# Kernel optimization log

Measured on AMD Instinct MI355X. Metric: run time of the kernel, lower is better.

The kernel has to match this reference:

```python
import jax, jax.numpy as jnp
import numpy as np

MODEL_DIM = 256
PAIR_IMPORTANCE_WEIGHT = 0.5
B, S, D = 4, 4096, MODEL_DIM


def setup_inputs() -> dict:
    key = jax.random.key(0)
    ks = jax.random.split(key, 6)
    return {
        "query": jax.random.normal(ks[0], (B, S, D), dtype=jnp.float32),
        "key": jax.random.normal(ks[1], (B, S, D), dtype=jnp.float32),
        "value": jax.random.normal(ks[2], (B, S, D), dtype=jnp.float32),
        "W_query": jax.random.normal(ks[3], (D, D), dtype=jnp.float32),
        "W_key": jax.random.normal(ks[4], (D, D), dtype=jnp.float32),
        "W_value": jax.random.normal(ks[5], (D, D), dtype=jnp.float32),
    }


def reference(query, key, value, W_query, W_key, W_value):
    # Projections: [B,S,D] @ [D,D]
    q = jnp.einsum('bsd,de->bse', query, W_query)
    k = jnp.einsum('bsd,de->bse', key, W_key)
    v = jnp.einsum('bsd,de->bse', value, W_value)
    scale = jnp.sqrt(jnp.asarray(MODEL_DIM, dtype=q.dtype))
    # Full [B,S,S] score matrix (global max forces materialization)
    scores = jnp.einsum('bqd,bkd->bqk', q, k) / scale
    s_len = scores.shape[1]
    diag_bias = jnp.eye(s_len, dtype=scores.dtype) * jnp.max(scores)
    scores = scores + PAIR_IMPORTANCE_WEIGHT * diag_bias  # broadcast over batch
    attention_weights = jax.nn.softmax(scores, axis=-1)
    output = jnp.einsum('bqk,bkd->bqd', attention_weights, v)
    return output, attention_weights
```

## Files before the change

kernel.cpp:

```cpp
#include <hip/hip_runtime.h>
#include <cstdint>
#include <cstddef>

#define BB 4
#define SS 4096
#define DD 256
#define PIW 0.5f
#define NROW (BB * SS)

typedef float          f32x4  __attribute__((ext_vector_type(4)));
typedef __bf16         bf16v8 __attribute__((ext_vector_type(8)));
typedef unsigned short u16v8  __attribute__((ext_vector_type(8)));
typedef unsigned short u16v4  __attribute__((ext_vector_type(4)));

__device__ __forceinline__ f32x4 mfma_bf16(u16v8 a, u16v8 b, f32x4 c) {
    return __builtin_amdgcn_mfma_f32_16x16x32_bf16(
        __builtin_bit_cast(bf16v8, a), __builtin_bit_cast(bf16v8, b), c, 0, 0, 0);
}

__device__ __forceinline__ unsigned short f2bf(float f) {
    unsigned u = __float_as_uint(f);
    u += 0x7FFFu + ((u >> 16) & 1u);
    return (unsigned short)(u >> 16);
}
__device__ __forceinline__ float bf2f(unsigned short h) {
    return __uint_as_float(((unsigned)h) << 16);
}
__device__ __forceinline__ unsigned fenc(float x) {
    unsigned u = __float_as_uint(x);
    return (u & 0x80000000u) ? ~u : (u | 0x80000000u);
}
__device__ __forceinline__ float fdec(unsigned e) {
    return __uint_as_float((e & 0x80000000u) ? (e ^ 0x80000000u) : ~e);
}

__device__ __forceinline__ void split8(float4 x0, float4 x1, u16v8* h, u16v8* l) {
    float xs[8] = {x0.x, x0.y, x0.z, x0.w, x1.x, x1.y, x1.z, x1.w};
    #pragma unroll
    for (int e = 0; e < 8; e++) {
        unsigned short hh = f2bf(xs[e]);
        (*h)[e] = hh;
        (*l)[e] = f2bf(xs[e] - bf2f(hh));
    }
}

#define FPAD 36

__global__ __launch_bounds__(256) void proj_mfma(
    const float* __restrict__ query, const float* __restrict__ key_, const float* __restrict__ value,
    const float* __restrict__ Wq, const float* __restrict__ Wk, const float* __restrict__ Wv,
    unsigned short* __restrict__ qh, unsigned short* __restrict__ ql,
    unsigned short* __restrict__ kh, unsigned short* __restrict__ kl,
    unsigned short* __restrict__ vT, unsigned* __restrict__ gmax)
{
    const int z = blockIdx.z;
    const float* A = (z == 0) ? query : (z == 1) ? key_ : value;
    const float* W = (z == 0) ? Wq    : (z == 1) ? Wk   : Wv;
    if (z == 0 && blockIdx.x == 0 && blockIdx.y == 0 && threadIdx.x == 0)
        *gmax = 0x007FFFFFu;

    __shared__ float Af[128][FPAD];
    __shared__ float Wf[128][FPAD];

    const int tid = threadIdx.x;
    const int lane = tid & 63, w = tid >> 6;
    const int wr = (w >> 1) * 64, wc = (w & 1) * 64;
    const int m = lane & 15, qq = lane >> 4;
    const int rowBase = blockIdx.y * 128;
    const int colBase = blockIdx.x * 128;

    f32x4 acc[4][4];
    #pragma unroll
    for (int i = 0; i < 4; i++)
        #pragma unroll
        for (int j = 0; j < 4; j++)
            acc[i][j] = (f32x4){0.f, 0.f, 0.f, 0.f};

    for (int k0 = 0; k0 < DD; k0 += 32) {
        #pragma unroll
        for (int i = 0; i < 4; i++) {
            int c = tid + i * 256;
            int r = c >> 3, q8 = c & 7;
            *(float4*)&Af[r][q8 * 4] = *(const float4*)&A[(size_t)(rowBase + r) * DD + k0 + q8 * 4];
        }
        {
            int c = tid & 127, kk0 = (tid >> 7) * 16;
            #pragma unroll
            for (int kk = 0; kk < 16; kk++)
                Wf[c][kk0 + kk] = W[(size_t)(k0 + kk0 + kk) * DD + colBase + c];
        }
        __syncthreads();

        u16v8 ah[4], al[4], bh[4], bl[4];
        #pragma unroll
        for (int i = 0; i < 4; i++) {
            float4 x0 = *(const float4*)&Af[wr + i * 16 + m][qq * 8];
            float4 x1 = *(const float4*)&Af[wr + i * 16 + m][qq * 8 + 4];
            split8(x0, x1, &ah[i], &al[i]);
        }
        #pragma unroll
        for (int j = 0; j < 4; j++) {
            float4 x0 = *(const float4*)&Wf[wc + j * 16 + m][qq * 8];
            float4 x1 = *(const float4*)&Wf[wc + j * 16 + m][qq * 8 + 4];
            split8(x0, x1, &bh[j], &bl[j]);
        }
        #pragma unroll
        for (int i = 0; i < 4; i++)
            #pragma unroll
            for (int j = 0; j < 4; j++) {
                acc[i][j] = mfma_bf16(ah[i], bh[j], acc[i][j]);
                acc[i][j] = mfma_bf16(ah[i], bl[j], acc[i][j]);
                acc[i][j] = mfma_bf16(al[i], bh[j], acc[i][j]);
            }
        __syncthreads();
    }

    #pragma unroll
    for (int i = 0; i < 4; i++) {
        #pragma unroll
        for (int j = 0; j < 4; j++) {
            #pragma unroll
            for (int r = 0; r < 4; r++) {
                int gr  = rowBase + wr + i * 16 + qq * 4 + r;
                int col = colBase + wc + j * 16 + m;
                float v = acc[i][j][r];
                if (z == 2) {
                    int b2 = gr >> 12, s2 = gr & (SS - 1);
                    vT[((size_t)b2 * DD + col) * SS + s2] = f2bf(v);
                } else {
                    if (z == 0) v *= (1.0f / 16.0f);
                    unsigned short hh = f2bf(v);
                    unsigned short ll = f2bf(v - bf2f(hh));
                    size_t idx = (size_t)gr * DD + col;
                    if (z == 0) { qh[idx] = hh; ql[idx] = ll; }
                    else        { kh[idx] = hh; kl[idx] = ll; }
                }
            }
        }
    }
}

#define SPAD 40

__global__ __launch_bounds__(256) void scores_mfma(
    const unsigned short* __restrict__ qh, const unsigned short* __restrict__ ql,
    const unsigned short* __restrict__ kh, const unsigned short* __restrict__ kl,
    float* __restrict__ attn, float* __restrict__ pmax, float* __restrict__ psum,
    unsigned* __restrict__ gmax)
{
    const int b = blockIdx.z;
    const size_t boff = (size_t)b * SS * DD;
    const unsigned short* Qh = qh + boff;
    const unsigned short* Ql = ql + boff;
    const unsigned short* Kh = kh + boff;
    const unsigned short* Kl = kl + boff;
    float* C = attn + (size_t)b * SS * SS;

    __shared__ unsigned short Ah[128][SPAD];
    __shared__ unsigned short Al[128][SPAD];
    __shared__ unsigned short Bh[128][SPAD];
    __shared__ unsigned short Bl[128][SPAD];
    __shared__ float smax[128][2];
    __shared__ float ssum[128][2];
    __shared__ float red[256];

    const int tid = threadIdx.x;
    const int lane = tid & 63, w = tid >> 6;
    const int wr = (w >> 1) * 64, wc = (w & 1) * 64;
    const int m = lane & 15, qq = lane >> 4;
    const int rowBase = blockIdx.y * 128;
    const int colBase = blockIdx.x * 128;

    f32x4 acc[4][4];
    #pragma unroll
    for (int i = 0; i < 4; i++)
        #pragma unroll
        for (int j = 0; j < 4; j++)
            acc[i][j] = (f32x4){0.f, 0.f, 0.f, 0.f};

    const int chunk = (tid & 3) * 8;
    const int srow  = tid >> 2;

    for (int k0 = 0; k0 < DD; k0 += 32) {
        #pragma unroll
        for (int i = 0; i < 2; i++) {
            int r = srow + i * 64;
            size_t ga = (size_t)(rowBase + r) * DD + k0 + chunk;
            size_t gb = (size_t)(colBase + r) * DD + k0 + chunk;
            *(u16v8*)&Ah[r][chunk] = *(const u16v8*)&Qh[ga];
            *(u16v8*)&Al[r][chunk] = *(const u16v8*)&Ql[ga];
            *(u16v8*)&Bh[r][chunk] = *(const u16v8*)&Kh[gb];
            *(u16v8*)&Bl[r][chunk] = *(const u16v8*)&Kl[gb];
        }
        __syncthreads();

        const int kb = qq * 8;
        u16v8 ah[4], al[4], bh[4], bl[4];
        #pragma unroll
        for (int i = 0; i < 4; i++) {
            ah[i] = *(const u16v8*)&Ah[wr + i * 16 + m][kb];
            al[i] = *(const u16v8*)&Al[wr + i * 16 + m][kb];
            bh[i] = *(const u16v8*)&Bh[wc + i * 16 + m][kb];
            bl[i] = *(const u16v8*)&Bl[wc + i * 16 + m][kb];
        }
        #pragma unroll
        for (int i = 0; i < 4; i++)
            #pragma unroll
            for (int j = 0; j < 4; j++) {
                acc[i][j] = mfma_bf16(ah[i], bh[j], acc[i][j]);
                acc[i][j] = mfma_bf16(ah[i], bl[j], acc[i][j]);
                acc[i][j] = mfma_bf16(al[i], bh[j], acc[i][j]);
            }
        __syncthreads();
    }

    float vm_all = -INFINITY;
    #pragma unroll
    for (int i = 0; i < 4; i++) {
        #pragma unroll
        for (int r = 0; r < 4; r++) {
            int row = rowBase + wr + i * 16 + qq * 4 + r;
            float vj[4];
            float vm = -INFINITY;
            #pragma unroll
            for (int j = 0; j < 4; j++) {
                vj[j] = acc[i][j][r];
                C[(size_t)row * SS + colBase + wc + j * 16 + m] = vj[j];
                vm = fmaxf(vm, vj[j]);
            }
            #pragma unroll
            for (int o = 1; o < 16; o <<= 1)
                vm = fmaxf(vm, __shfl_xor(vm, o));
            float vs = 0.f;
            #pragma unroll
            for (int j = 0; j < 4; j++)
                vs += __expf(vj[j] - vm);
            #pragma unroll
            for (int o = 1; o < 16; o <<= 1)
                vs += __shfl_xor(vs, o);
            vm_all = fmaxf(vm_all, vm);
            if (m == 0) {
                smax[wr + i * 16 + qq * 4 + r][w & 1] = vm;
                ssum[wr + i * 16 + qq * 4 + r][w & 1] = vs;
            }
        }
    }
    red[tid] = vm_all;
    __syncthreads();
    if (tid < 128) {
        float m0 = smax[tid][0], m1 = smax[tid][1];
        float M = fmaxf(m0, m1);
        float P = ssum[tid][0] * __expf(m0 - M) + ssum[tid][1] * __expf(m1 - M);
        size_t idx = (size_t)blockIdx.x * NROW + (b * SS + rowBase + tid);
        pmax[idx] = M;
        psum[idx] = P;
    }
    for (int s2 = 128; s2 > 0; s2 >>= 1) {
        if (tid < s2) red[tid] = fmaxf(red[tid], red[tid + s2]);
        __syncthreads();
    }
    if (tid == 0) atomicMax(gmax, fenc(red[0]));
}

__global__ __launch_bounds__(256) void combine_kernel(
    const float* __restrict__ pmax, const float* __restrict__ psum,
    const float* __restrict__ attn, const unsigned* __restrict__ gmax,
    float* __restrict__ rmax, float* __restrict__ rinv)
{
    const int row = blockIdx.x * 256 + threadIdx.x;
    const int b = row >> 12, i = row & (SS - 1);
    const float bias = PIW * fdec(*gmax);
    const float d = attn[(size_t)b * SS * SS + (size_t)i * SS + i];

    float M = -INFINITY;
    #pragma unroll 8
    for (int t = 0; t < 32; t++) M = fmaxf(M, pmax[(size_t)t * NROW + row]);
    const float db = d + bias;
    const float Mrow = fmaxf(M, db);
    const int t0 = i >> 7;
    float S = 0.f;
    #pragma unroll 8
    for (int t = 0; t < 32; t++) {
        float pm = pmax[(size_t)t * NROW + row];
        float P  = psum[(size_t)t * NROW + row];
        if (t == t0) P -= __expf(d - pm);
        S += P * __expf(pm - Mrow);
    }
    S += __expf(db - Mrow);
    rmax[row] = Mrow;
    rinv[row] = 1.0f / S;
}

#define VPAD 72

__global__ __launch_bounds__(512) void av_fused2(
    float* __restrict__ attn, const unsigned short* __restrict__ vT,
    const float* __restrict__ rmax, const float* __restrict__ rinv,
    const unsigned* __restrict__ gmax, float* __restrict__ out)
{
    const int b = blockIdx.y;
    const int rowBase = blockIdx.x * 64;
    float* A = attn + (size_t)b * SS * SS;
    const unsigned short* Bv = vT + (size_t)b * DD * SS;
    const float bias = PIW * fdec(*gmax);

    __shared__ unsigned short P[2][64][VPAD];
    __shared__ unsigned short V[2][256][VPAD];
    __shared__ float sM[64], sI[64];

    const int tid = threadIdx.x;
    const int lane = tid & 63, w = tid >> 6;
    const int m = lane & 15, qq = lane >> 4;

    if (tid < 64) {
        sM[tid] = rmax[b * SS + rowBase + tid];
        sI[tid] = rinv[b * SS + rowBase + tid];
    }

    const int pr = tid >> 3, pc = (tid & 7) * 8;
    const int vr = tid >> 1, vc = (tid & 1) * 32;
    const size_t rawRow = (size_t)(rowBase + pr) * SS;
    const size_t vRow   = (size_t)vr * SS;
    const int growDiag  = rowBase + pr;

    float4 ra0 = *(const float4*)&A[rawRow + pc];
    float4 ra1 = *(const float4*)&A[rawRow + pc + 4];
    u16v8 rv[4];
    #pragma unroll
    for (int u = 0; u < 4; u++)
        rv[u] = *(const u16v8*)&Bv[vRow + vc + u * 8];
    __syncthreads();

    f32x4 acc[4][2];
    #pragma unroll
    for (int i = 0; i < 4; i++)
        #pragma unroll
        for (int j = 0; j < 2; j++)
            acc[i][j] = (f32x4){0.f, 0.f, 0.f, 0.f};

    const float Mr = sM[pr], Ir = sI[pr];

    int cur = 0;
    for (int ct = 0; ct < SS / 64; ct++) {
        const int kc = ct * 64;
        {
            float xs[8] = {ra0.x, ra0.y, ra0.z, ra0.w, ra1.x, ra1.y, ra1.z, ra1.w};
            float wv[8];
            #pragma unroll
            for (int e = 0; e < 8; e++) {
                float s = xs[e] + ((kc + pc + e == growDiag) ? bias : 0.f);
                wv[e] = __expf(s - Mr) * Ir;
            }
            *(float4*)&A[rawRow + kc + pc]     = make_float4(wv[0], wv[1], wv[2], wv[3]);
            *(float4*)&A[rawRow + kc + pc + 4] = make_float4(wv[4], wv[5], wv[6], wv[7]);
            *(u16v4*)&P[cur][pr][pc]     = (u16v4){f2bf(wv[0]), f2bf(wv[1]), f2bf(wv[2]), f2bf(wv[3])};
            *(u16v4*)&P[cur][pr][pc + 4] = (u16v4){f2bf(wv[4]), f2bf(wv[5]), f2bf(wv[6]), f2bf(wv[7])};
            #pragma unroll
            for (int u = 0; u < 4; u++)
                *(u16v8*)&V[cur][vr][vc + u * 8] = rv[u];
        }
        __syncthreads();

        if (ct + 1 < SS / 64) {
            const int kn = kc + 64;
            ra0 = *(const float4*)&A[rawRow + kn + pc];
            ra1 = *(const float4*)&A[rawRow + kn + pc + 4];
            #pragma unroll
            for (int u = 0; u < 4; u++)
                rv[u] = *(const u16v8*)&Bv[vRow + kn + vc + u * 8];
        }

        #pragma unroll
        for (int kk = 0; kk < 64; kk += 32) {
            u16v8 af[4], bf[2];
            #pragma unroll
            for (int i = 0; i < 4; i++)
                af[i] = *(const u16v8*)&P[cur][i * 16 + m][kk + qq * 8];
            #pragma unroll
            for (int j = 0; j < 2; j++)
                bf[j] = *(const u16v8*)&V[cur][w * 32 + j * 16 + m][kk + qq * 8];
            #pragma unroll
            for (int i = 0; i < 4; i++)
                #pragma unroll
                for (int j = 0; j < 2; j++)
                    acc[i][j] = mfma_bf16(af[i], bf[j], acc[i][j]);
        }
        cur ^= 1;
    }

    #pragma unroll
    for (int i = 0; i < 4; i++) {
        #pragma unroll
        for (int j = 0; j < 2; j++) {
            #pragma unroll
            for (int rr = 0; rr < 4; rr++) {
                int row = rowBase + i * 16 + qq * 4 + rr;
                int col = w * 32 + j * 16 + m;
                out[((size_t)b * SS + row) * DD + col] = acc[i][j][rr];
            }
        }
    }
}

extern "C" void kernel_launch(void* const* d_in, const int* in_sizes, int n_in,
                              void* d_out, int out_size, void* d_ws, size_t ws_size,
                              hipStream_t stream)
{
    const float* query = (const float*)d_in[0];
    const float* key_  = (const float*)d_in[1];
    const float* value = (const float*)d_in[2];
    const float* Wq    = (const float*)d_in[3];
    const float* Wk    = (const float*)d_in[4];
    const float* Wv    = (const float*)d_in[5];

    float* out  = (float*)d_out;
    float* attn = out + (size_t)BB * SS * DD;

    const size_t E = (size_t)BB * SS * DD;
    unsigned short* qh = (unsigned short*)d_ws;
    unsigned short* ql = qh + E;
    unsigned short* kh = ql + E;
    unsigned short* kl = kh + E;
    unsigned short* vT = kl + E;
    float* pmax = (float*)(vT + E);
    float* psum = pmax + (size_t)32 * NROW;
    float* rmax = psum + (size_t)32 * NROW;
    float* rinv = rmax + NROW;
    unsigned* gmax = (unsigned*)(rinv + NROW);

    proj_mfma<<<dim3(DD / 128, NROW / 128, 3), 256, 0, stream>>>(
        query, key_, value, Wq, Wk, Wv, qh, ql, kh, kl, vT, gmax);
    scores_mfma<<<dim3(SS / 128, SS / 128, BB), 256, 0, stream>>>(
        qh, ql, kh, kl, attn, pmax, psum, gmax);
    combine_kernel<<<dim3(NROW / 256), 256, 0, stream>>>(
        pmax, psum, attn, gmax, rmax, rinv);
    av_fused2<<<dim3(SS / 64, BB), 512, 0, stream>>>(
        attn, vT, rmax, rinv, gmax, out);
}
```

Measured before the change: 708.6 us.

## Replace LDS-staged attention-times-V kernel with per-wave register MFMA kernel

Rewrites the final normalize-and-multiply kernel so each wave owns 16 rows and feeds its normalized probabilities straight from registers into MFMA, with no shared memory or block barriers. V fragments are loaded directly from global memory for all 256 output columns. This removes the LDS staging and __syncthreads traffic. In exchange, V is no longer shared through LDS, so each wave rereads it from global/L2, and the global V reads are strided gathers.

```diff
diff --git a/kernel.cpp b/kernel.cpp
--- a/kernel.cpp
+++ b/kernel.cpp
@@ -291,113 +291,67 @@
     rinv[row] = 1.0f / S;
 }
 
-#define VPAD 72
-
-__global__ __launch_bounds__(512) void av_fused2(
+__global__ __launch_bounds__(256) void av_wave(
     float* __restrict__ attn, const unsigned short* __restrict__ vT,
     const float* __restrict__ rmax, const float* __restrict__ rinv,
     const unsigned* __restrict__ gmax, float* __restrict__ out)
 {
     const int b = blockIdx.y;
-    const int rowBase = blockIdx.x * 64;
+    const int tid = threadIdx.x;
+    const int lane = tid & 63, w = tid >> 6;
+    const int m = lane & 15, qq = lane >> 4;
+    const int waveRow = blockIdx.x * 64 + w * 16;
+    const int row = waveRow + m;
+
     float* A = attn + (size_t)b * SS * SS;
     const unsigned short* Bv = vT + (size_t)b * DD * SS;
     const float bias = PIW * fdec(*gmax);
-
-    __shared__ unsigned short P[2][64][VPAD];
-    __shared__ unsigned short V[2][256][VPAD];
-    __shared__ float sM[64], sI[64];
-
-    const int tid = threadIdx.x;
-    const int lane = tid & 63, w = tid >> 6;
-    const int m = lane & 15, qq = lane >> 4;
-
-    if (tid < 64) {
-        sM[tid] = rmax[b * SS + rowBase + tid];
-        sI[tid] = rinv[b * SS + rowBase + tid];
-    }
-
-    const int pr = tid >> 3, pc = (tid & 7) * 8;
-    const int vr = tid >> 1, vc = (tid & 1) * 32;
-    const size_t rawRow = (size_t)(rowBase + pr) * SS;
-    const size_t vRow   = (size_t)vr * SS;
-    const int growDiag  = rowBase + pr;
-
-    float4 ra0 = *(const float4*)&A[rawRow + pc];
-    float4 ra1 = *(const float4*)&A[rawRow + pc + 4];
-    u16v8 rv[4];
-    #pragma unroll
-    for (int u = 0; u < 4; u++)
-        rv[u] = *(const u16v8*)&Bv[vRow + vc + u * 8];
-    __syncthreads();
-
-    f32x4 acc[4][2];
-    #pragma unroll
-    for (int i = 0; i < 4; i++)
-        #pragma unroll
-        for (int j = 0; j < 2; j++)
-            acc[i][j] = (f32x4){0.f, 0.f, 0.f, 0.f};
-
-    const float Mr = sM[pr], Ir = sI[pr];
-
-    int cur = 0;
-    for (int ct = 0; ct < SS / 64; ct++) {
-        const int kc = ct * 64;
-        {
-            float xs[8] = {ra0.x, ra0.y, ra0.z, ra0.w, ra1.x, ra1.y, ra1.z, ra1.w};
-            float wv[8];
-            #pragma unroll
-            for (int e = 0; e < 8; e++) {
-                float s = xs[e] + ((kc + pc + e == growDiag) ? bias : 0.f);
-                wv[e] = __expf(s - Mr) * Ir;
-            }
-            *(float4*)&A[rawRow + kc + pc]     = make_float4(wv[0], wv[1], wv[2], wv[3]);
-            *(float4*)&A[rawRow + kc + pc + 4] = make_float4(wv[4], wv[5], wv[6], wv[7]);
-            *(u16v4*)&P[cur][pr][pc]     = (u16v4){f2bf(wv[0]), f2bf(wv[1]), f2bf(wv[2]), f2bf(wv[3])};
-            *(u16v4*)&P[cur][pr][pc + 4] = (u16v4){f2bf(wv[4]), f2bf(wv[5]), f2bf(wv[6]), f2bf(wv[7])};
-            #pragma unroll
-            for (int u = 0; u < 4; u++)
-                *(u16v8*)&V[cur][vr][vc + u * 8] = rv[u];
-        }
-        __syncthreads();
-
-        if (ct + 1 < SS / 64) {
-            const int kn = kc + 64;
-            ra0 = *(const float4*)&A[rawRow + kn + pc];
-            ra1 = *(const float4*)&A[rawRow + kn + pc + 4];
-            #pragma unroll
-            for (int u = 0; u < 4; u++)
-                rv[u] = *(const u16v8*)&Bv[vRow + kn + vc + u * 8];
-        }
-
-        #pragma unroll
-        for (int kk = 0; kk < 64; kk += 32) {
-            u16v8 af[4], bf[2];
-            #pragma unroll
-            for (int i = 0; i < 4; i++)
-                af[i] = *(const u16v8*)&P[cur][i * 16 + m][kk + qq * 8];
-            #pragma unroll
-            for (int j = 0; j < 2; j++)
-                bf[j] = *(const u16v8*)&V[cur][w * 32 + j * 16 + m][kk + qq * 8];
-            #pragma unroll
-            for (int i = 0; i < 4; i++)
-                #pragma unroll
-                for (int j = 0; j < 2; j++)
-                    acc[i][j] = mfma_bf16(af[i], bf[j], acc[i][j]);
-        }
-        cur ^= 1;
-    }
-
-    #pragma unroll
-    for (int i = 0; i < 4; i++) {
-        #pragma unroll
-        for (int j = 0; j < 2; j++) {
-            #pragma unroll
-            for (int rr = 0; rr < 4; rr++) {
-                int row = rowBase + i * 16 + qq * 4 + rr;
-                int col = w * 32 + j * 16 + m;
-                out[((size_t)b * SS + row) * DD + col] = acc[i][j][rr];
-            }
+    const float Mr = rmax[b * SS + row];
+    const float Ir = rinv[b * SS + row];
+
+    const size_t rawOff = (size_t)row * SS + qq * 8;
+    const int kOff = qq * 8;
+
+    f32x4 acc[16];
+    #pragma unroll
+    for (int j = 0; j < 16; j++)
+        acc[j] = (f32x4){0.f, 0.f, 0.f, 0.f};
+
+    float4 r0 = *(const float4*)&A[rawOff];
+    float4 r1 = *(const float4*)&A[rawOff + 4];
+
+    for (int kc = 0; kc < SS; kc += 32) {
+        float xs[8] = {r0.x, r0.y, r0.z, r0.w, r1.x, r1.y, r1.z, r1.w};
+        if (kc + 32 < SS) {
+            r0 = *(const float4*)&A[rawOff + kc + 32];
+            r1 = *(const float4*)&A[rawOff + kc + 36];
+        }
+        float wv[8];
+        #pragma unroll
+        for (int e = 0; e < 8; e++) {
+            float s = xs[e] + ((kc + kOff + e == row) ? bias : 0.f);
+            wv[e] = __expf(s - Mr) * Ir;
+        }
+        *(float4*)&A[rawOff + kc]     = make_float4(wv[0], wv[1], wv[2], wv[3]);
+        *(float4*)&A[rawOff + kc + 4] = make_float4(wv[4], wv[5], wv[6], wv[7]);
+        u16v8 af;
+        #pragma unroll
+        for (int e = 0; e < 8; e++) af[e] = f2bf(wv[e]);
+
+        #pragma unroll
+        for (int j = 0; j < 16; j++) {
+            u16v8 bf = *(const u16v8*)&Bv[(size_t)(j * 16 + m) * SS + kc + kOff];
+            acc[j] = mfma_bf16(af, bf, acc[j]);
+        }
+    }
+
+    #pragma unroll
+    for (int j = 0; j < 16; j++) {
+        #pragma unroll
+        for (int rr = 0; rr < 4; rr++) {
+            int orow = waveRow + qq * 4 + rr;
+            int ocol = j * 16 + m;
+            out[((size_t)b * SS + orow) * DD + ocol] = acc[j][rr];
         }
     }
 }
@@ -434,6 +388,6 @@
         qh, ql, kh, kl, attn, pmax, psum, gmax);
     combine_kernel<<<dim3(NROW / 256), 256, 0, stream>>>(
         pmax, psum, attn, gmax, rmax, rinv);
-    av_fused2<<<dim3(SS / 64, BB), 512, 0, stream>>>(
+    av_wave<<<dim3(SS / 64, BB), 256, 0, stream>>>(
         attn, vT, rmax, rinv, gmax, out);
 }
```

New measurement: 1.016 ms. +43.4%, slower.
